# Kernel tuning notes

Measured on AMD Instinct MI355X. Metric: run time of the kernel, lower is better.

Reference implementation:

```python
import jax, jax.numpy as jnp
import numpy as np

B, S, D, H = 2, 2048, 1024, 16
DK = D // H
MAX_REL = 2047          # clip range for relative distances
REL_DIM = 64            # rel_embedding dim, summed over


def setup_inputs() -> dict:
    key = jax.random.key(0)
    ks = jax.random.split(key, 12)
    sc = 1.0 / np.sqrt(D)
    inp = {
        "q": jax.random.normal(ks[0], (B, S, D), jnp.float32),
        "k": jax.random.normal(ks[1], (B, S, D), jnp.float32),
        "v": jax.random.normal(ks[2], (B, S, D), jnp.float32),
        "Wq": jax.random.normal(ks[3], (D, D), jnp.float32) * sc,
        "bq": jnp.zeros((D,), jnp.float32),
        "Wk": jax.random.normal(ks[4], (D, D), jnp.float32) * sc,
        "bk": jnp.zeros((D,), jnp.float32),
        "Wv": jax.random.normal(ks[5], (D, D), jnp.float32) * sc,
        "bv": jnp.zeros((D,), jnp.float32),
        "Wo": jax.random.normal(ks[6], (D, D), jnp.float32) * sc,
        "bo": jnp.zeros((D,), jnp.float32),
        "rel_table": jax.random.normal(ks[7], (2 * MAX_REL + 1, REL_DIM), jnp.float32) * 0.02,
        "mask": jnp.tril(jnp.ones((1, 1, S, S), jnp.bool_)),  # causal
    }
    return inp


def reference(q, k, v, Wq, bq, Wk, bk, Wv, bv, Wo, bo, rel_table, mask):
    def split_heads(x):
        # [B,S,D] -> [B,H,S,DK]
        return x.reshape(B, -1, H, DK).transpose(0, 2, 1, 3)

    Q = split_heads(q @ Wq + bq)
    K = split_heads(k @ Wk + bk)
    V = split_heads(v @ Wv + bv)

    scores = jnp.einsum("bhqd,bhkd->bhqk", Q, K) / jnp.sqrt(jnp.float32(DK))

    # relative position bias: table[clip(j - i)] summed over rel dim -> [S,S]
    rel_idx = jnp.clip(jnp.arange(S)[None, :] - jnp.arange(S)[:, None],
                       -MAX_REL, MAX_REL) + MAX_REL
    rel_bias = rel_table[rel_idx].sum(-1)  # [S,S]
    scores = scores + rel_bias[None, None]

    scores = jnp.where(mask, scores, jnp.float32(-1e20))
    attn = jax.nn.softmax(scores, axis=-1)

    out = jnp.einsum("bhqk,bhkd->bhqd", attn, V)
    out = out.transpose(0, 2, 1, 3).reshape(B, -1, D)
    return out @ Wo + bo
```

## Files before the change

kernel.cpp:

```cpp
#include <hip/hip_runtime.h>

#define SEQ 2048
#define DIM 1024
#define NH 16
#define HD 64
#define NB 2

typedef __bf16 bf16x8 __attribute__((ext_vector_type(8)));
typedef float f32x4 __attribute__((ext_vector_type(4)));
typedef float f32x4v __attribute__((ext_vector_type(4)));
typedef float f32x4u __attribute__((ext_vector_type(4), aligned(4)));
typedef unsigned short us8 __attribute__((ext_vector_type(8)));
typedef unsigned short us4 __attribute__((ext_vector_type(4)));

#define LOG2E 1.44269504f

__device__ __forceinline__ unsigned short bfbits(float f) {
  __bf16 h = (__bf16)f;
  return __builtin_bit_cast(unsigned short, h);
}

__global__ void relsum_kernel(const float* __restrict__ rel_table,
                              float* __restrict__ relsum) {
  int i = blockIdx.x * blockDim.x + threadIdx.x;
  if (i < 4095) {
    const f32x4v* row = reinterpret_cast<const f32x4v*>(rel_table + (size_t)i * 64);
    float s = 0.f;
    for (int d = 0; d < 16; ++d) {
      f32x4v v = row[d];
      s += v[0] + v[1] + v[2] + v[3];
    }
    relsum[i] = s * LOG2E;
  }
}

__global__ __launch_bounds__(256) void wconv4_kernel(
    const float* __restrict__ W0, const float* __restrict__ W1,
    const float* __restrict__ W2, const float* __restrict__ W3,
    unsigned short* __restrict__ Wt) {
  __shared__ unsigned short T[64][68];
  int z = blockIdx.z;
  const float* W = (z == 0) ? W0 : (z == 1) ? W1 : (z == 2) ? W2 : W3;
  unsigned short* out = Wt + (size_t)z * 1024 * 1024;
  int r0 = blockIdx.y * 64;
  int c0 = blockIdx.x * 64;
  int tid = threadIdx.x;
  for (int it = 0; it < 4; ++it) {
    int s = tid + it * 256;
    int r = s >> 4;
    int c4 = (s & 15) * 4;
    f32x4v v = *reinterpret_cast<const f32x4v*>(W + (size_t)(r0 + r) * 1024 + c0 + c4);
    us4 o;
    o[0] = bfbits(v[0]); o[1] = bfbits(v[1]); o[2] = bfbits(v[2]); o[3] = bfbits(v[3]);
    *reinterpret_cast<us4*>(&T[r][c4]) = o;
  }
  __syncthreads();
  for (int it = 0; it < 2; ++it) {
    int s = tid + it * 256;
    int n = s >> 3;
    int k8 = (s & 7) * 8;
    us8 o;
    for (int e = 0; e < 8; ++e) o[e] = T[k8 + e][n];
    *reinterpret_cast<us8*>(out + (size_t)(c0 + n) * 1024 + r0 + k8) = o;
  }
}

__global__ __launch_bounds__(256) void vtrans_kernel(
    const unsigned short* __restrict__ Vb, unsigned short* __restrict__ Vt) {
  __shared__ unsigned short T[64 * 72];
  int s0 = blockIdx.x * 64;
  int h = blockIdx.y;
  int b = blockIdx.z;
  int tid = threadIdx.x;
  int key0 = tid >> 3;
  int cg0 = (tid & 7) * 8;
  int j0 = tid & 7;
  const unsigned short* src = Vb + ((size_t)(b * SEQ + s0)) * DIM + h * HD;
  for (int it = 0; it < 2; ++it) {
    int key = key0 + it * 32;
    us8 v = *reinterpret_cast<const us8*>(src + (size_t)key * DIM + cg0);
    for (int e = 0; e < 8; ++e) {
      unsigned idx = (unsigned)((cg0 + e) * 72 + key) ^ ((unsigned)j0 << 3);
      T[idx] = v[e];
    }
  }
  __syncthreads();
  for (int it = 0; it < 2; ++it) {
    int slot = tid + it * 256;
    int dk = slot >> 3;
    int k8 = (slot & 7) * 8;
    unsigned idx = ((unsigned)(dk * 72 + k8)) ^ ((((unsigned)dk >> 3) & 7u) << 3);
    us8 o = *reinterpret_cast<const us8*>(&T[idx]);
    *reinterpret_cast<us8*>(Vt + ((size_t)(b * NH + h) * HD + dk) * SEQ + s0 + k8) = o;
  }
}

__global__ __launch_bounds__(256) void gemm_qkv_kernel(
    const float* __restrict__ Aq, const float* __restrict__ Ak,
    const float* __restrict__ Av, const unsigned short* __restrict__ WTb,
    const float* __restrict__ bq, const float* __restrict__ bk,
    const float* __restrict__ bv, unsigned short* __restrict__ Qb,
    unsigned short* __restrict__ Kb, unsigned short* __restrict__ Vb,
    float qscale) {
  constexpr int N = 1024, K = 1024;
  int o = (blockIdx.x & 7) * 192 + (blockIdx.x >> 3);
  int row0 = (o / 48) * 128;
  int colz = o % 48;
  int z = colz >> 4;
  int col0 = (colz & 15) * 64;
  const float* A = (z == 0) ? Aq : (z == 1) ? Ak : Av;
  const unsigned short* WT = WTb + (size_t)z * N * K;
  const float* bias = (z == 0) ? bq : (z == 1) ? bk : bv;
  unsigned short* Cp = (z == 0) ? Qb : (z == 1) ? Kb : Vb;
  float oscale = (z == 0) ? qscale : 1.0f;

  int tid = threadIdx.x;
  int w = tid >> 6;
  int lane = tid & 63;
  int lg = lane >> 4;
  int li = lane & 15;
  int wr = (w >> 1) * 64;
  int wc = (w & 1) * 32;

  __shared__ unsigned short As[2][128][72];
  __shared__ unsigned short Ws[2][64][72];

  f32x4v af32[8];
  us8 wreg[2];

#define GLOAD(KS)                                                         \
  {                                                                       \
    int k0 = (KS) * 64;                                                   \
    for (int it = 0; it < 8; ++it) {                                      \
      int s = tid + it * 256;                                             \
      int r = s >> 4;                                                     \
      int cg = (s & 15) * 4;                                              \
      af32[it] = *reinterpret_cast<const f32x4v*>(                        \
          A + (size_t)(row0 + r) * K + k0 + cg);                          \
    }                                                                     \
    for (int it = 0; it < 2; ++it) {                                      \
      int s = tid + it * 256;                                             \
      int c = s >> 3;                                                     \
      int kg = (s & 7) * 8;                                               \
      wreg[it] = *reinterpret_cast<const us8*>(                           \
          WT + (size_t)(col0 + c) * K + k0 + kg);                         \
    }                                                                     \
  }

#define SWRITE(B)                                                         \
  {                                                                       \
    for (int it = 0; it < 8; ++it) {                                      \
      int s = tid + it * 256;                                             \
      int r = s >> 4;                                                     \
      int cg = (s & 15) * 4;                                              \
      us4 o2;                                                             \
      o2[0] = bfbits(af32[it][0]); o2[1] = bfbits(af32[it][1]);           \
      o2[2] = bfbits(af32[it][2]); o2[3] = bfbits(af32[it][3]);           \
      *reinterpret_cast<us4*>(&As[B][r][cg]) = o2;                        \
    }                                                                     \
    for (int it = 0; it < 2; ++it) {                                      \
      int s = tid + it * 256;                                             \
      int c = s >> 3;                                                     \
      int kg = (s & 7) * 8;                                               \
      *reinterpret_cast<us8*>(&Ws[B][c][kg]) = wreg[it];                  \
    }                                                                     \
  }

  f32x4 acc[4][2] = {};

  GLOAD(0);
  SWRITE(0);
  GLOAD(1);
  __syncthreads();

  for (int ks = 0; ks < 16; ++ks) {
    if (ks < 15) SWRITE((ks + 1) & 1);
    if (ks < 14) GLOAD(ks + 2);
    int B = ks & 1;
    for (int kk = 0; kk < 2; ++kk) {
      bf16x8 af[4], bfr[2];
      for (int m = 0; m < 4; ++m)
        af[m] = *reinterpret_cast<const bf16x8*>(&As[B][wr + m * 16 + li][kk * 32 + lg * 8]);
      for (int n = 0; n < 2; ++n)
        bfr[n] = *reinterpret_cast<const bf16x8*>(&Ws[B][wc + n * 16 + li][kk * 32 + lg * 8]);
      for (int m = 0; m < 4; ++m)
        for (int n = 0; n < 2; ++n)
          acc[m][n] = __builtin_amdgcn_mfma_f32_16x16x32_bf16(af[m], bfr[n], acc[m][n], 0, 0, 0);
    }
    __syncthreads();
  }

  for (int m = 0; m < 4; ++m)
    for (int n = 0; n < 2; ++n)
      for (int r = 0; r < 4; ++r) {
        int row = row0 + wr + m * 16 + lg * 4 + r;
        int col = col0 + wc + n * 16 + li;
        float val = (acc[m][n][r] + bias[col]) * oscale;
        Cp[(size_t)row * N + col] = bfbits(val);
      }
#undef GLOAD
#undef SWRITE
}

__global__ __launch_bounds__(256) void gemm_out_kernel(
    const unsigned short* __restrict__ A, const unsigned short* __restrict__ WT,
    const float* __restrict__ bias, float* __restrict__ Cp) {
  constexpr int N = 1024, K = 1024;
  int o = ((blockIdx.x & 7) << 6) | (blockIdx.x >> 3);
  int col0 = (o & 15) * 64;
  int row0 = (o >> 4) * 128;
  int tid = threadIdx.x;
  int w = tid >> 6;
  int lane = tid & 63;
  int lg = lane >> 4;
  int li = lane & 15;
  int wr = (w >> 1) * 64;
  int wc = (w & 1) * 32;

  __shared__ unsigned short As[2][128][72];
  __shared__ unsigned short Ws[2][64][72];

  us8 ab16[4];
  us8 wreg[2];

#define GLOAD(KS)                                                         \
  {                                                                       \
    int k0 = (KS) * 64;                                                   \
    for (int it = 0; it < 4; ++it) {                                      \
      int s = tid + it * 256;                                             \
      int r = s >> 3;                                                     \
      int cg = (s & 7) * 8;                                               \
      ab16[it] = *reinterpret_cast<const us8*>(                           \
          A + (size_t)(row0 + r) * K + k0 + cg);                          \
    }                                                                     \
    for (int it = 0; it < 2; ++it) {                                      \
      int s = tid + it * 256;                                             \
      int c = s >> 3;                                                     \
      int kg = (s & 7) * 8;                                               \
      wreg[it] = *reinterpret_cast<const us8*>(                           \
          WT + (size_t)(col0 + c) * K + k0 + kg);                         \
    }                                                                     \
  }

#define SWRITE(B)                                                         \
  {                                                                       \
    for (int it = 0; it < 4; ++it) {                                      \
      int s = tid + it * 256;                                             \
      int r = s >> 3;                                                     \
      int cg = (s & 7) * 8;                                               \
      *reinterpret_cast<us8*>(&As[B][r][cg]) = ab16[it];                  \
    }                                                                     \
    for (int it = 0; it < 2; ++it) {                                      \
      int s = tid + it * 256;                                             \
      int c = s >> 3;                                                     \
      int kg = (s & 7) * 8;                                               \
      *reinterpret_cast<us8*>(&Ws[B][c][kg]) = wreg[it];                  \
    }                                                                     \
  }

  f32x4 acc[4][2] = {};

  GLOAD(0);
  SWRITE(0);
  GLOAD(1);
  __syncthreads();

  for (int ks = 0; ks < 16; ++ks) {
    if (ks < 15) SWRITE((ks + 1) & 1);
    if (ks < 14) GLOAD(ks + 2);
    int B = ks & 1;
    for (int kk = 0; kk < 2; ++kk) {
      bf16x8 af[4], bfr[2];
      for (int m = 0; m < 4; ++m)
        af[m] = *reinterpret_cast<const bf16x8*>(&As[B][wr + m * 16 + li][kk * 32 + lg * 8]);
      for (int n = 0; n < 2; ++n)
        bfr[n] = *reinterpret_cast<const bf16x8*>(&Ws[B][wc + n * 16 + li][kk * 32 + lg * 8]);
      for (int m = 0; m < 4; ++m)
        for (int n = 0; n < 2; ++n)
          acc[m][n] = __builtin_amdgcn_mfma_f32_16x16x32_bf16(af[m], bfr[n], acc[m][n], 0, 0, 0);
    }
    __syncthreads();
  }

  for (int m = 0; m < 4; ++m)
    for (int n = 0; n < 2; ++n)
      for (int r = 0; r < 4; ++r) {
        int row = row0 + wr + m * 16 + lg * 4 + r;
        int col = col0 + wc + n * 16 + li;
        Cp[(size_t)row * N + col] = acc[m][n][r] + bias[col];
      }
#undef GLOAD
#undef SWRITE
}

__global__ __launch_bounds__(256) void attn_kernel(
    const unsigned short* __restrict__ Qb, const unsigned short* __restrict__ Kb,
    const unsigned short* __restrict__ Vt, const float* __restrict__ relsum,
    unsigned short* __restrict__ Ob) {
  int o = ((blockIdx.x & 7) << 6) | (blockIdx.x >> 3);
  int p = o & 15;
  int h = (o >> 4) & 15;
  int b = o >> 8;

  int tid = threadIdx.x;
  int w = tid >> 6;
  int lane = tid & 63;
  int lg = lane >> 4;
  int li = lane & 15;

  __shared__ unsigned short Ks[64][72];
  __shared__ unsigned short VtF[64 * 72];
  __shared__ __bf16 Ps[4][16][72];
  __shared__ float rel_lds[2112];

  for (int it = 0; it < 3; ++it) {
    int slot = tid + it * 256;
    if (slot < 528)
      *reinterpret_cast<f32x4v*>(&rel_lds[slot * 4]) =
          *reinterpret_cast<const f32x4v*>(&relsum[slot * 4]);
  }

  int key0 = tid >> 3;
  int cg0 = (tid & 7) * 8;
  int dk0 = tid >> 3;
  int k8 = (tid & 7) * 8;
  const unsigned short* kptr = Kb + ((size_t)(b * SEQ + key0)) * DIM + h * HD + cg0;
  const unsigned short* vtp = Vt + ((size_t)(b * NH + h) * HD + dk0) * SEQ + k8;

  unsigned vidx0 = ((unsigned)(dk0 * 72 + k8)) ^ ((((unsigned)dk0 >> 3) & 7u) << 3);
  unsigned vidx1 = ((unsigned)((dk0 + 32) * 72 + k8)) ^
                   ((((unsigned)(dk0 + 32) >> 3) & 7u) << 3);

  us8 krg0, krg1, vrg0, vrg1;

#define LOAD_REGS(TT)                                                     \
  {                                                                       \
    size_t koff = (size_t)(TT) * 64 * DIM;                                \
    krg0 = *reinterpret_cast<const us8*>(kptr + koff);                    \
    krg1 = *reinterpret_cast<const us8*>(kptr + koff + 32 * DIM);         \
    vrg0 = *reinterpret_cast<const us8*>(vtp + (TT) * 64);                \
    vrg1 = *reinterpret_cast<const us8*>(vtp + 32 * SEQ + (TT) * 64);     \
  }

#define WRITE_TILE()                                                      \
  {                                                                       \
    *reinterpret_cast<us8*>(&Ks[key0][cg0]) = krg0;                       \
    *reinterpret_cast<us8*>(&Ks[key0 + 32][cg0]) = krg1;                  \
    *reinterpret_cast<us8*>(&VtF[vidx0]) = vrg0;                          \
    *reinterpret_cast<us8*>(&VtF[vidx1]) = vrg1;                          \
  }

  LOAD_REGS(0);

  for (int ph = 0; ph < 2; ++ph) {
    int qt = ph ? p : (31 - p);

    int qrow = qt * 64 + w * 16 + li;
    const unsigned short* qb = Qb + ((size_t)(b * SEQ + qrow)) * DIM + h * HD;
    bf16x8 qa0 = *reinterpret_cast<const bf16x8*>(qb + lg * 8);
    bf16x8 qa1 = *reinterpret_cast<const bf16x8*>(qb + 32 + lg * 8);

    f32x4 o_acc[4] = {};
    float m_row[4], l_row[4];
    for (int r = 0; r < 4; ++r) { m_row[r] = -3e38f; l_row[r] = 0.f; }
    int i0 = qt * 64 + w * 16 + lg * 4;

    for (int t = 0; t <= qt; ++t) {
      __syncthreads();
      WRITE_TILE();
      __syncthreads();

      if (!(ph == 1 && t == qt)) {
        int nextT = (t < qt) ? (t + 1) : 0;
        LOAD_REGS(nextT);
      }

      f32x4 s_acc[4] = {};
      __builtin_amdgcn_s_setprio(1);
      for (int kk = 0; kk < 2; ++kk) {
        bf16x8 qa = kk ? qa1 : qa0;
        for (int n = 0; n < 4; ++n) {
          bf16x8 kb = *reinterpret_cast<const bf16x8*>(&Ks[n * 16 + li][kk * 32 + lg * 8]);
          s_acc[n] = __builtin_amdgcn_mfma_f32_16x16x32_bf16(qa, kb, s_acc[n], 0, 0, 0);
        }
      }
      __builtin_amdgcn_s_setprio(0);

      float tmax[4] = {-3e38f, -3e38f, -3e38f, -3e38f};
      int Cbase = (t - qt) * 64 - (w * 16 + lg * 4) + li + 2047;
      if (t == qt) {
        for (int n = 0; n < 4; ++n) {
          int Cn = Cbase + n * 16;
          f32x4u rel4 = *reinterpret_cast<const f32x4u*>(&rel_lds[Cn - 3]);
          for (int r = 0; r < 4; ++r) {
            float sv = s_acc[n][r] + rel4[3 - r];
            sv = (Cn - r > 2047) ? -1e30f : sv;
            s_acc[n][r] = sv;
            tmax[r] = fmaxf(tmax[r], sv);
          }
        }
      } else {
        for (int n = 0; n < 4; ++n) {
          int Cn = Cbase + n * 16;
          f32x4u rel4 = *reinterpret_cast<const f32x4u*>(&rel_lds[Cn - 3]);
          for (int r = 0; r < 4; ++r) {
            float sv = s_acc[n][r] + rel4[3 - r];
            s_acc[n][r] = sv;
            tmax[r] = fmaxf(tmax[r], sv);
          }
        }
      }

      bool okl = true;
      for (int r = 0; r < 4; ++r) okl &= (tmax[r] <= m_row[r] + 8.f);
      if (!__all(okl)) {
        for (int msk = 1; msk < 16; msk <<= 1)
          for (int r = 0; r < 4; ++r)
            tmax[r] = fmaxf(tmax[r], __shfl_xor(tmax[r], msk));
        for (int r = 0; r < 4; ++r) {
          float mn = fmaxf(m_row[r], tmax[r]);
          float al = exp2f(m_row[r] - mn);
          m_row[r] = mn;
          l_row[r] *= al;
          o_acc[0][r] *= al; o_acc[1][r] *= al;
          o_acc[2][r] *= al; o_acc[3][r] *= al;
        }
      }

      for (int n = 0; n < 4; ++n)
        for (int r = 0; r < 4; ++r) {
          float e = exp2f(s_acc[n][r] - m_row[r]);
          s_acc[n][r] = e;
          l_row[r] += e;
        }

      for (int n = 0; n < 4; ++n)
        for (int r = 0; r < 4; ++r)
          Ps[w][lg * 4 + r][n * 16 + li] = (__bf16)s_acc[n][r];
      asm volatile("s_waitcnt lgkmcnt(0)" ::: "memory");
      __builtin_amdgcn_sched_barrier(0);

      __builtin_amdgcn_s_setprio(1);
      for (int kk = 0; kk < 2; ++kk) {
        bf16x8 pa = *reinterpret_cast<const bf16x8*>(&Ps[w][li][kk * 32 + lg * 8]);
        for (int n = 0; n < 4; ++n) {
          int dk = n * 16 + li;
          unsigned idx = ((unsigned)(dk * 72 + kk * 32 + lg * 8)) ^
                         ((((unsigned)dk >> 3) & 7u) << 3);
          bf16x8 vb = *reinterpret_cast<const bf16x8*>(&VtF[idx]);
          o_acc[n] = __builtin_amdgcn_mfma_f32_16x16x32_bf16(pa, vb, o_acc[n], 0, 0, 0);
        }
      }
      __builtin_amdgcn_s_setprio(0);
    }

    for (int msk = 1; msk < 16; msk <<= 1)
      for (int r = 0; r < 4; ++r) l_row[r] += __shfl_xor(l_row[r], msk);
    float inv_l[4];
    for (int r = 0; r < 4; ++r) inv_l[r] = 1.f / l_row[r];
    for (int n = 0; n < 4; ++n)
      for (int r = 0; r < 4; ++r) {
        int row = i0 + r;
        int dk = n * 16 + li;
        Ob[((size_t)(b * SEQ + row)) * DIM + h * HD + dk] =
            bfbits(o_acc[n][r] * inv_l[r]);
      }
  }
#undef LOAD_REGS
#undef WRITE_TILE
}

extern "C" void kernel_launch(void* const* d_in, const int* in_sizes, int n_in,
                              void* d_out, int out_size, void* d_ws, size_t ws_size,
                              hipStream_t stream) {
  const float* q = (const float*)d_in[0];
  const float* k = (const float*)d_in[1];
  const float* v = (const float*)d_in[2];
  const float* Wq = (const float*)d_in[3];
  const float* bq = (const float*)d_in[4];
  const float* Wk = (const float*)d_in[5];
  const float* bk = (const float*)d_in[6];
  const float* Wv = (const float*)d_in[7];
  const float* bv = (const float*)d_in[8];
  const float* Wo = (const float*)d_in[9];
  const float* bo = (const float*)d_in[10];
  const float* rel = (const float*)d_in[11];

  char* ws = (char*)d_ws;
  const size_t MATB = (size_t)NB * SEQ * DIM * sizeof(unsigned short);
  const size_t WTE = (size_t)DIM * DIM;
  unsigned short* Qb = (unsigned short*)(ws);
  unsigned short* Kb = (unsigned short*)(ws + MATB);
  unsigned short* Vb = (unsigned short*)(ws + 2 * MATB);
  unsigned short* Ob = (unsigned short*)(ws + 3 * MATB);
  float* relsum = (float*)(ws + 4 * MATB);
  unsigned short* WT = (unsigned short*)(ws + 4 * MATB + 65536);
  unsigned short* Vt = (unsigned short*)(ws + 4 * MATB + 65536 + 4 * WTE * 2);

  relsum_kernel<<<16, 256, 0, stream>>>(rel, relsum);
  wconv4_kernel<<<dim3(16, 16, 4), 256, 0, stream>>>(Wq, Wk, Wv, Wo, WT);

  const float qscale = 0.125f * LOG2E;
  gemm_qkv_kernel<<<dim3(1536), 256, 0, stream>>>(q, k, v, WT, bq, bk, bv,
                                                  Qb, Kb, Vb, qscale);
  vtrans_kernel<<<dim3(SEQ / 64, NH, NB), 256, 0, stream>>>(Vb, Vt);

  attn_kernel<<<dim3(512), 256, 0, stream>>>(Qb, Kb, Vt, relsum, Ob);

  gemm_out_kernel<<<dim3(512), 256, 0, stream>>>(Ob, WT + 3 * WTE, bo, (float*)d_out);
}
```

Baseline: 141.1 us.

## Fuse V transpose into QKV GEMM, merge relsum, widen attention KV tiles

The QKV GEMM now writes V directly in the transposed per-head layout, which removes the separate vtrans kernel and its round trip through memory. The relsum computation becomes an extra z-slice of the weight conversion kernel, saving one launch. The attention kernel processes 128-key tiles instead of 64, halving loop iterations and barriers at the cost of more LDS and registers. The wider tiles also waste causal-masked work on the diagonal tile.

```diff
diff --git a/kernel.cpp b/kernel.cpp
--- a/kernel.cpp
+++ b/kernel.cpp
@@ -20,31 +20,32 @@
   return __builtin_bit_cast(unsigned short, h);
 }
 
-__global__ void relsum_kernel(const float* __restrict__ rel_table,
-                              float* __restrict__ relsum) {
-  int i = blockIdx.x * blockDim.x + threadIdx.x;
-  if (i < 4095) {
-    const f32x4v* row = reinterpret_cast<const f32x4v*>(rel_table + (size_t)i * 64);
-    float s = 0.f;
-    for (int d = 0; d < 16; ++d) {
-      f32x4v v = row[d];
-      s += v[0] + v[1] + v[2] + v[3];
-    }
-    relsum[i] = s * LOG2E;
-  }
-}
-
 __global__ __launch_bounds__(256) void wconv4_kernel(
     const float* __restrict__ W0, const float* __restrict__ W1,
     const float* __restrict__ W2, const float* __restrict__ W3,
-    unsigned short* __restrict__ Wt) {
+    unsigned short* __restrict__ Wt, const float* __restrict__ rel_table,
+    float* __restrict__ relsum) {
+  int z = blockIdx.z;
+  int tid = threadIdx.x;
+  if (z == 4) {
+    int ti = blockIdx.y * 16 + blockIdx.x;
+    int i = ti * 256 + tid;
+    if (i < 4095) {
+      const f32x4v* row = reinterpret_cast<const f32x4v*>(rel_table + (size_t)i * 64);
+      float s = 0.f;
+      for (int d = 0; d < 16; ++d) {
+        f32x4v v = row[d];
+        s += v[0] + v[1] + v[2] + v[3];
+      }
+      relsum[i] = s * LOG2E;
+    }
+    return;
+  }
   __shared__ unsigned short T[64][68];
-  int z = blockIdx.z;
   const float* W = (z == 0) ? W0 : (z == 1) ? W1 : (z == 2) ? W2 : W3;
   unsigned short* out = Wt + (size_t)z * 1024 * 1024;
   int r0 = blockIdx.y * 64;
   int c0 = blockIdx.x * 64;
-  int tid = threadIdx.x;
   for (int it = 0; it < 4; ++it) {
     int s = tid + it * 256;
     int r = s >> 4;
@@ -65,42 +66,12 @@
   }
 }
 
-__global__ __launch_bounds__(256) void vtrans_kernel(
-    const unsigned short* __restrict__ Vb, unsigned short* __restrict__ Vt) {
-  __shared__ unsigned short T[64 * 72];
-  int s0 = blockIdx.x * 64;
-  int h = blockIdx.y;
-  int b = blockIdx.z;
-  int tid = threadIdx.x;
-  int key0 = tid >> 3;
-  int cg0 = (tid & 7) * 8;
-  int j0 = tid & 7;
-  const unsigned short* src = Vb + ((size_t)(b * SEQ + s0)) * DIM + h * HD;
-  for (int it = 0; it < 2; ++it) {
-    int key = key0 + it * 32;
-    us8 v = *reinterpret_cast<const us8*>(src + (size_t)key * DIM + cg0);
-    for (int e = 0; e < 8; ++e) {
-      unsigned idx = (unsigned)((cg0 + e) * 72 + key) ^ ((unsigned)j0 << 3);
-      T[idx] = v[e];
-    }
-  }
-  __syncthreads();
-  for (int it = 0; it < 2; ++it) {
-    int slot = tid + it * 256;
-    int dk = slot >> 3;
-    int k8 = (slot & 7) * 8;
-    unsigned idx = ((unsigned)(dk * 72 + k8)) ^ ((((unsigned)dk >> 3) & 7u) << 3);
-    us8 o = *reinterpret_cast<const us8*>(&T[idx]);
-    *reinterpret_cast<us8*>(Vt + ((size_t)(b * NH + h) * HD + dk) * SEQ + s0 + k8) = o;
-  }
-}
-
 __global__ __launch_bounds__(256) void gemm_qkv_kernel(
     const float* __restrict__ Aq, const float* __restrict__ Ak,
     const float* __restrict__ Av, const unsigned short* __restrict__ WTb,
     const float* __restrict__ bq, const float* __restrict__ bk,
     const float* __restrict__ bv, unsigned short* __restrict__ Qb,
-    unsigned short* __restrict__ Kb, unsigned short* __restrict__ Vb,
+    unsigned short* __restrict__ Kb, unsigned short* __restrict__ Vt,
     float qscale) {
   constexpr int N = 1024, K = 1024;
   int o = (blockIdx.x & 7) * 192 + (blockIdx.x >> 3);
@@ -111,7 +82,6 @@
   const float* A = (z == 0) ? Aq : (z == 1) ? Ak : Av;
   const unsigned short* WT = WTb + (size_t)z * N * K;
   const float* bias = (z == 0) ? bq : (z == 1) ? bk : bv;
-  unsigned short* Cp = (z == 0) ? Qb : (z == 1) ? Kb : Vb;
   float oscale = (z == 0) ? qscale : 1.0f;
 
   int tid = threadIdx.x;
@@ -191,13 +161,25 @@
   }
 
   for (int m = 0; m < 4; ++m)
-    for (int n = 0; n < 2; ++n)
-      for (int r = 0; r < 4; ++r) {
-        int row = row0 + wr + m * 16 + lg * 4 + r;
-        int col = col0 + wc + n * 16 + li;
-        float val = (acc[m][n][r] + bias[col]) * oscale;
-        Cp[(size_t)row * N + col] = bfbits(val);
-      }
+    for (int n = 0; n < 2; ++n) {
+      int row = row0 + wr + m * 16 + lg * 4;
+      int col = col0 + wc + n * 16 + li;
+      float v4[4];
+      for (int r = 0; r < 4; ++r) v4[r] = (acc[m][n][r] + bias[col]) * oscale;
+      if (z == 2) {
+        int bb = row >> 11, seq = row & 2047;
+        int hh = col >> 6, dk = col & 63;
+        us4 o4;
+        o4[0] = bfbits(v4[0]); o4[1] = bfbits(v4[1]);
+        o4[2] = bfbits(v4[2]); o4[3] = bfbits(v4[3]);
+        *reinterpret_cast<us4*>(
+            Vt + ((size_t)(bb * NH + hh) * HD + dk) * SEQ + seq) = o4;
+      } else {
+        unsigned short* Cp = (z == 0) ? Qb : Kb;
+        for (int r = 0; r < 4; ++r)
+          Cp[(size_t)(row + r) * N + col] = bfbits(v4[r]);
+      }
+    }
 #undef GLOAD
 #undef SWRITE
 }
@@ -308,14 +290,14 @@
   int lg = lane >> 4;
   int li = lane & 15;
 
-  __shared__ unsigned short Ks[64][72];
-  __shared__ unsigned short VtF[64 * 72];
-  __shared__ __bf16 Ps[4][16][72];
-  __shared__ float rel_lds[2112];
+  __shared__ unsigned short Ks[128][72];
+  __shared__ unsigned short VtF[2][64 * 72];
+  __shared__ __bf16 Ps[4][16][136];
+  __shared__ float rel_lds[2176];
 
   for (int it = 0; it < 3; ++it) {
     int slot = tid + it * 256;
-    if (slot < 528)
+    if (slot < 544)
       *reinterpret_cast<f32x4v*>(&rel_lds[slot * 4]) =
           *reinterpret_cast<const f32x4v*>(&relsum[slot * 4]);
   }
@@ -331,29 +313,38 @@
   unsigned vidx1 = ((unsigned)((dk0 + 32) * 72 + k8)) ^
                    ((((unsigned)(dk0 + 32) >> 3) & 7u) << 3);
 
-  us8 krg0, krg1, vrg0, vrg1;
+  us8 krg[4], vrg[4];
 
 #define LOAD_REGS(TT)                                                     \
   {                                                                       \
-    size_t koff = (size_t)(TT) * 64 * DIM;                                \
-    krg0 = *reinterpret_cast<const us8*>(kptr + koff);                    \
-    krg1 = *reinterpret_cast<const us8*>(kptr + koff + 32 * DIM);         \
-    vrg0 = *reinterpret_cast<const us8*>(vtp + (TT) * 64);                \
-    vrg1 = *reinterpret_cast<const us8*>(vtp + 32 * SEQ + (TT) * 64);     \
-  }
-
-#define WRITE_TILE()                                                      \
-  {                                                                       \
-    *reinterpret_cast<us8*>(&Ks[key0][cg0]) = krg0;                       \
-    *reinterpret_cast<us8*>(&Ks[key0 + 32][cg0]) = krg1;                  \
-    *reinterpret_cast<us8*>(&VtF[vidx0]) = vrg0;                          \
-    *reinterpret_cast<us8*>(&VtF[vidx1]) = vrg1;                          \
+    size_t koff = (size_t)(TT) * 128 * DIM;                               \
+    krg[0] = *reinterpret_cast<const us8*>(kptr + koff);                  \
+    krg[1] = *reinterpret_cast<const us8*>(kptr + koff + 32 * DIM);       \
+    krg[2] = *reinterpret_cast<const us8*>(kptr + koff + 64 * DIM);       \
+    krg[3] = *reinterpret_cast<const us8*>(kptr + koff + 96 * DIM);       \
+    vrg[0] = *reinterpret_cast<const us8*>(vtp + (TT) * 128);             \
+    vrg[1] = *reinterpret_cast<const us8*>(vtp + 32 * SEQ + (TT) * 128);  \
+    vrg[2] = *reinterpret_cast<const us8*>(vtp + (TT) * 128 + 64);        \
+    vrg[3] = *reinterpret_cast<const us8*>(vtp + 32 * SEQ + (TT) * 128 + 64); \
+  }
+
+#define WRITE_TILE()                                                     \
+  {                                                                      \
+    *reinterpret_cast<us8*>(&Ks[key0][cg0]) = krg[0];                    \
+    *reinterpret_cast<us8*>(&Ks[key0 + 32][cg0]) = krg[1];               \
+    *reinterpret_cast<us8*>(&Ks[key0 + 64][cg0]) = krg[2];               \
+    *reinterpret_cast<us8*>(&Ks[key0 + 96][cg0]) = krg[3];               \
+    *reinterpret_cast<us8*>(&VtF[0][vidx0]) = vrg[0];                    \
+    *reinterpret_cast<us8*>(&VtF[0][vidx1]) = vrg[1];                    \
+    *reinterpret_cast<us8*>(&VtF[1][vidx0]) = vrg[2];                    \
+    *reinterpret_cast<us8*>(&VtF[1][vidx1]) = vrg[3];                    \
   }
 
   LOAD_REGS(0);
 
   for (int ph = 0; ph < 2; ++ph) {
     int qt = ph ? p : (31 - p);
+    int nkv = (qt + 2) >> 1;
 
     int qrow = qt * 64 + w * 16 + li;
     const unsigned short* qb = Qb + ((size_t)(b * SEQ + qrow)) * DIM + h * HD;
@@ -365,21 +356,21 @@
     for (int r = 0; r < 4; ++r) { m_row[r] = -3e38f; l_row[r] = 0.f; }
     int i0 = qt * 64 + w * 16 + lg * 4;
 
-    for (int t = 0; t <= qt; ++t) {
+    for (int t = 0; t < nkv; ++t) {
       __syncthreads();
       WRITE_TILE();
       __syncthreads();
 
-      if (!(ph == 1 && t == qt)) {
-        int nextT = (t < qt) ? (t + 1) : 0;
+      if (!(ph == 1 && t == nkv - 1)) {
+        int nextT = (t + 1 < nkv) ? (t + 1) : 0;
         LOAD_REGS(nextT);
       }
 
-      f32x4 s_acc[4] = {};
+      f32x4 s_acc[8] = {};
       __builtin_amdgcn_s_setprio(1);
       for (int kk = 0; kk < 2; ++kk) {
         bf16x8 qa = kk ? qa1 : qa0;
-        for (int n = 0; n < 4; ++n) {
+        for (int n = 0; n < 8; ++n) {
           bf16x8 kb = *reinterpret_cast<const bf16x8*>(&Ks[n * 16 + li][kk * 32 + lg * 8]);
           s_acc[n] = __builtin_amdgcn_mfma_f32_16x16x32_bf16(qa, kb, s_acc[n], 0, 0, 0);
         }
@@ -387,9 +378,9 @@
       __builtin_amdgcn_s_setprio(0);
 
       float tmax[4] = {-3e38f, -3e38f, -3e38f, -3e38f};
-      int Cbase = (t - qt) * 64 - (w * 16 + lg * 4) + li + 2047;
-      if (t == qt) {
-        for (int n = 0; n < 4; ++n) {
+      int Cbase = t * 128 - (qt * 64 + w * 16 + lg * 4) + li + 2047;
+      if (t == nkv - 1) {
+        for (int n = 0; n < 8; ++n) {
           int Cn = Cbase + n * 16;
           f32x4u rel4 = *reinterpret_cast<const f32x4u*>(&rel_lds[Cn - 3]);
           for (int r = 0; r < 4; ++r) {
@@ -400,7 +391,7 @@
           }
         }
       } else {
-        for (int n = 0; n < 4; ++n) {
+        for (int n = 0; n < 8; ++n) {
           int Cn = Cbase + n * 16;
           f32x4u rel4 = *reinterpret_cast<const f32x4u*>(&rel_lds[Cn - 3]);
           for (int r = 0; r < 4; ++r) {
@@ -427,27 +418,29 @@
         }
       }
 
-      for (int n = 0; n < 4; ++n)
+      for (int n = 0; n < 8; ++n)
         for (int r = 0; r < 4; ++r) {
           float e = exp2f(s_acc[n][r] - m_row[r]);
           s_acc[n][r] = e;
           l_row[r] += e;
         }
 
-      for (int n = 0; n < 4; ++n)
+      for (int n = 0; n < 8; ++n)
         for (int r = 0; r < 4; ++r)
           Ps[w][lg * 4 + r][n * 16 + li] = (__bf16)s_acc[n][r];
       asm volatile("s_waitcnt lgkmcnt(0)" ::: "memory");
       __builtin_amdgcn_sched_barrier(0);
 
       __builtin_amdgcn_s_setprio(1);
-      for (int kk = 0; kk < 2; ++kk) {
-        bf16x8 pa = *reinterpret_cast<const bf16x8*>(&Ps[w][li][kk * 32 + lg * 8]);
+      for (int kstep = 0; kstep < 4; ++kstep) {
+        int half = kstep >> 1;
+        int kk = kstep & 1;
+        bf16x8 pa = *reinterpret_cast<const bf16x8*>(&Ps[w][li][kstep * 32 + lg * 8]);
         for (int n = 0; n < 4; ++n) {
           int dk = n * 16 + li;
           unsigned idx = ((unsigned)(dk * 72 + kk * 32 + lg * 8)) ^
                          ((((unsigned)dk >> 3) & 7u) << 3);
-          bf16x8 vb = *reinterpret_cast<const bf16x8*>(&VtF[idx]);
+          bf16x8 vb = *reinterpret_cast<const bf16x8*>(&VtF[half][idx]);
           o_acc[n] = __builtin_amdgcn_mfma_f32_16x16x32_bf16(pa, vb, o_acc[n], 0, 0, 0);
         }
       }
@@ -491,19 +484,16 @@
   const size_t WTE = (size_t)DIM * DIM;
   unsigned short* Qb = (unsigned short*)(ws);
   unsigned short* Kb = (unsigned short*)(ws + MATB);
-  unsigned short* Vb = (unsigned short*)(ws + 2 * MATB);
+  unsigned short* Vt = (unsigned short*)(ws + 2 * MATB);
   unsigned short* Ob = (unsigned short*)(ws + 3 * MATB);
   float* relsum = (float*)(ws + 4 * MATB);
   unsigned short* WT = (unsigned short*)(ws + 4 * MATB + 65536);
-  unsigned short* Vt = (unsigned short*)(ws + 4 * MATB + 65536 + 4 * WTE * 2);
-
-  relsum_kernel<<<16, 256, 0, stream>>>(rel, relsum);
-  wconv4_kernel<<<dim3(16, 16, 4), 256, 0, stream>>>(Wq, Wk, Wv, Wo, WT);
+
+  wconv4_kernel<<<dim3(16, 16, 5), 256, 0, stream>>>(Wq, Wk, Wv, Wo, WT, rel, relsum);
 
   const float qscale = 0.125f * LOG2E;
   gemm_qkv_kernel<<<dim3(1536), 256, 0, stream>>>(q, k, v, WT, bq, bk, bv,
-                                                  Qb, Kb, Vb, qscale);
-  vtrans_kernel<<<dim3(SEQ / 64, NH, NB), 256, 0, stream>>>(Vb, Vt);
+                                                  Qb, Kb, Vt, qscale);
 
   attn_kernel<<<dim3(512), 256, 0, stream>>>(Qb, Kb, Vt, relsum, Ob);
 
```

New measurement: 144.4 us. 1.02x slower.
